# Optimization experiments

Hardware: AMD Instinct MI355X
Metric: run time of the kernel (lower is better)

Reference implementation:

```python
import jax, jax.numpy as jnp
import numpy as np

N_A, N_B, D = 200_000, 400_000, 128
E1, E2 = 800_000, 800_000
UPDATE_KEEP = 0.5   # update_keep_prob
FEAT_KEEP = 0.3     # feature_keep_prob
LN_EPS = 1e-5


def setup_inputs() -> dict:
    key = jax.random.key(0)
    ks = jax.random.split(key, 22)
    s = 0.05  # weight scale
    f32 = jnp.float32
    return {
        "feats_A": jax.random.normal(ks[0], (N_A, D), f32),
        "feats_B": jax.random.normal(ks[1], (N_B, D), f32),
        "W_p2c": jax.random.normal(ks[2], (D, D), f32) * s,
        "b_p2c": jnp.zeros((D,), f32),
        "W_c2p": jax.random.normal(ks[3], (D, D), f32) * s,
        "b_c2p": jnp.zeros((D,), f32),
        "Wself_A": jax.random.normal(ks[4], (D, D), f32) * s,
        "bself_A": jnp.zeros((D,), f32),
        "lnw_A": jnp.ones((D,), f32),
        "lnb_A": jnp.zeros((D,), f32),
        "Wself_B": jax.random.normal(ks[5], (D, D), f32) * s,
        "bself_B": jnp.zeros((D,), f32),
        "lnw_B": jnp.ones((D,), f32),
        "lnb_B": jnp.zeros((D,), f32),
        "u_p2c": jax.random.uniform(ks[6], (E1, 1), f32),
        "u_c2p": jax.random.uniform(ks[7], (E2, 1), f32),
        "u_feat_A": jax.random.uniform(ks[8], (D,), f32),
        "u_feat_B": jax.random.uniform(ks[9], (D,), f32),
        "src_p2c": jax.random.randint(ks[10], (E1,), 0, N_A, jnp.int32),
        "dst_p2c": jax.random.randint(ks[11], (E1,), 0, N_B, jnp.int32),
        "src_c2p": jax.random.randint(ks[12], (E2,), 0, N_B, jnp.int32),
        "dst_c2p": jax.random.randint(ks[13], (E2,), 0, N_A, jnp.int32),
    }


def _edge_aggregate(src_feat, src_idx, dst_idx, W, b, u_edge, n_dst):
    # gather -> per-edge-type linear -> bernoulli update mask -> scatter-add
    msg = src_feat[src_idx] @ W.T + b                     # [E, D]
    um = (u_edge < UPDATE_KEEP).astype(src_feat.dtype)    # [E, 1]
    msg = msg * um
    agg = jax.ops.segment_sum(msg, dst_idx, num_segments=n_dst)       # [n_dst, D]
    deg = jax.ops.segment_sum(um[:, 0], dst_idx, num_segments=n_dst)  # [n_dst]
    return agg, deg


def _table_update(feats, agg, deg, Wself, bself, lnw, lnb, u_feat):
    deg = jnp.maximum(deg, 1.0)[:, None]
    fmask = (u_feat < FEAT_KEEP).astype(feats.dtype)      # [D], bernoulli(0.3)
    agg = (agg / deg) * fmask
    comb = feats @ Wself.T + bself + agg
    mu = jnp.mean(comb, axis=-1, keepdims=True)
    var = jnp.var(comb, axis=-1, keepdims=True)
    comb = (comb - mu) * jax.lax.rsqrt(var + LN_EPS) * lnw + lnb
    comb = jax.nn.selu(comb + feats)                      # residual (Identity proj) + SELU
    # write back only masked feature columns
    return jnp.where(fmask > 0.5, comb, feats)


def reference(feats_A, feats_B, W_p2c, b_p2c, W_c2p, b_c2p,
              Wself_A, bself_A, lnw_A, lnb_A,
              Wself_B, bself_B, lnw_B, lnb_B,
              u_p2c, u_c2p, u_feat_A, u_feat_B,
              src_p2c, dst_p2c, src_c2p, dst_c2p):
    # PARENT_TO_CHILD: A -> B ; CHILD_TO_PARENT: B -> A
    agg_B, deg_B = _edge_aggregate(feats_A, src_p2c, dst_p2c, W_p2c, b_p2c, u_p2c, N_B)
    agg_A, deg_A = _edge_aggregate(feats_B, src_c2p, dst_c2p, W_c2p, b_c2p, u_c2p, N_A)
    out_A = _table_update(feats_A, agg_A, deg_A, Wself_A, bself_A, lnw_A, lnb_A, u_feat_A)
    out_B = _table_update(feats_B, agg_B, deg_B, Wself_B, bself_B, lnw_B, lnb_B, u_feat_B)
    return (out_A, out_B)
```

## Files before the change

### kernel.cpp

```cpp
#include <hip/hip_runtime.h>
#include <hip/hip_bf16.h>

#define DD 128

typedef __attribute__((ext_vector_type(8))) short short8;
typedef __attribute__((ext_vector_type(8))) unsigned short u16x8;
typedef __attribute__((ext_vector_type(4))) unsigned short u16x4;
typedef __attribute__((ext_vector_type(4))) float f32x4;

__device__ __forceinline__ unsigned short f2bf(float f) {
    union { unsigned int u; float f; } c; c.f = f;
    unsigned int u = c.u;
    unsigned int r = (u + 0x7FFFu + ((u >> 16) & 1u)) >> 16;
    return (unsigned short)r;
}
__device__ __forceinline__ float bf2f(unsigned short h) {
    union { unsigned int u; float f; } c; c.u = ((unsigned int)h) << 16; return c.f;
}

__device__ __forceinline__ void scatter_dir(const float* __restrict__ feats,
                                            const int* __restrict__ src,
                                            const int* __restrict__ dst,
                                            const float* __restrict__ u,
                                            unsigned int* __restrict__ pre,
                                            float* __restrict__ deg,
                                            int E, int wave, int lane, int nw)
{
    for (int e = wave; e < E; e += nw) {
        if (u[e] < 0.5f) {
            int s = src[e], d = dst[e];
            float2 x = *(const float2*)(feats + (size_t)s * DD + 2 * lane);
            unsigned int* p = pre + (size_t)d * 64 + lane;
#if defined(__HIP_DEVICE_COMPILE__)
            typedef short sv2 __attribute__((ext_vector_type(2)));
            sv2 v; v[0] = (short)f2bf(x.x); v[1] = (short)f2bf(x.y);
            __builtin_amdgcn_global_atomic_fadd_v2bf16((__attribute__((address_space(1))) sv2*)p, v);
#else
            (void)p; (void)x;
#endif
            if (lane == 0) unsafeAtomicAdd(deg + d, 1.0f);
        }
    }
}

__global__ void scatter2_kernel(const float* __restrict__ f1,
                                const int* __restrict__ s1, const int* __restrict__ d1,
                                const float* __restrict__ u1,
                                unsigned int* __restrict__ p1, float* __restrict__ g1, int E1,
                                const float* __restrict__ f2,
                                const int* __restrict__ s2, const int* __restrict__ d2,
                                const float* __restrict__ u2,
                                unsigned int* __restrict__ p2, float* __restrict__ g2, int E2)
{
    int half = gridDim.x >> 1;
    int lane = threadIdx.x & 63;
    int wavein = (blockIdx.x % half) * (blockDim.x >> 6) + (threadIdx.x >> 6);
    int nw = half * (blockDim.x >> 6);
    if (blockIdx.x < half) scatter_dir(f1, s1, d1, u1, p1, g1, E1, wavein, lane, nw);
    else                   scatter_dir(f2, s2, d2, u2, p2, g2, E2, wavein, lane, nw);
}

__global__ __launch_bounds__(512, 2)
void table_kernel(const float* __restrict__ feats,
                  const unsigned short* __restrict__ pre,
                  const float* __restrict__ deg,
                  const float* __restrict__ Wself,
                  const float* __restrict__ bself,
                  const float* __restrict__ Wedge,
                  const float* __restrict__ bedge,
                  const float* __restrict__ lnw,
                  const float* __restrict__ lnb,
                  const float* __restrict__ ufeat,
                  float* __restrict__ out,
                  int N)
{
    __shared__ __align__(16) unsigned short wlds[2 * 16384];
    __shared__ __align__(16) char xsall[8 * 8192];

    const int tid = threadIdx.x;

    {
        int j  = tid >> 2;
        int kq = tid & 3;
        float fm = ufeat[j] < 0.3f ? 1.0f : 0.0f;
        const float* wsrow = Wself + j * DD + kq * 32;
        const float* werow = Wedge + j * DD + kq * 32;
        char* lbs = (char*)wlds;
        #pragma unroll
        for (int c = 0; c < 4; ++c) {
            unsigned short tS[8], tE[8];
            #pragma unroll
            for (int i = 0; i < 8; ++i) {
                tS[i] = f2bf(wsrow[c * 8 + i]);
                tE[i] = f2bf(werow[c * 8 + i] * fm);
            }
            int addr = (j * 256 + kq * 64 + c * 16) ^ ((j & 7) << 4);
            *(short8*)(lbs + addr)         = *(short8*)tS;
            *(short8*)(lbs + 32768 + addr) = *(short8*)tE;
        }
    }
    __syncthreads();

    const int wave = tid >> 6;
    const int lane = tid & 63;
    const int lj = lane & 15;
    const int lk = lane >> 4;

    float bs[8], bem[8], lw[8], lb[8];
    unsigned fmask = 0;
    #pragma unroll
    for (int ct = 0; ct < 8; ++ct) {
        int col = ct * 16 + lj;
        bool fm = ufeat[col] < 0.3f;
        bs[ct]  = bself[col];
        bem[ct] = fm ? bedge[col] : 0.0f;
        lw[ct]  = lnw[col];
        lb[ct]  = lnb[col];
        fmask |= (fm ? 1u : 0u) << ct;
    }

    char* xs  = xsall + wave * 8192;
    char* ps  = xs + 4096;
    const char* wb = (const char*)wlds;
    const int ldb  = lj * 256 + lk * 16;
    const int xorv = (lj & 7) << 4;

    const int frow = lane >> 5;
    const int fc4  = lane & 31;
    const int prow = lane >> 4;
    const int pch  = lane & 15;

    const int ntiles = N >> 4;
    for (int tile = blockIdx.x * 8 + wave; tile < ntiles; tile += gridDim.x * 8) {
        int row0 = tile << 4;

        #pragma unroll
        for (int j = 0; j < 8; ++j) {
            int row = j * 2 + frow;
            f32x4 v = __builtin_nontemporal_load(
                (const f32x4*)(feats + (size_t)(row0 + row) * DD + fc4 * 4));
            unsigned short t4[4];
            #pragma unroll
            for (int i = 0; i < 4; ++i) t4[i] = f2bf(v[i]);
            *(u16x4*)(xs + row * 256 + ((fc4 * 8) ^ ((row & 7) << 4))) = *(u16x4*)t4;
        }
        #pragma unroll
        for (int c = 0; c < 4; ++c) {
            int row = c * 4 + prow;
            u16x8 v = __builtin_nontemporal_load(
                (const u16x8*)(pre + (size_t)(row0 + row) * DD + pch * 8));
            *(u16x8*)(ps + row * 256 + ((pch * 16) ^ ((row & 7) << 4))) = v;
        }

        float dgr  = deg[row0 + lj];
        float invd = 1.0f / fmaxf(dgr, 1.0f);
        float dpown = dgr > 0.5f ? 1.0f : 0.0f;

        short8 xf[4], pf[4];
        #pragma unroll
        for (int t = 0; t < 4; ++t) {
            int a = (ldb + t * 64) ^ xorv;
            xf[t] = *(const short8*)(xs + a);
            u16x8 pv = *(const u16x8*)(ps + a);
            unsigned short tp[8];
            #pragma unroll
            for (int i = 0; i < 8; ++i) tp[i] = f2bf(bf2f(pv[i]) * invd);
            pf[t] = *(short8*)tp;
        }

        f32x4 acc[8];
        #pragma unroll
        for (int ct = 0; ct < 8; ++ct) { f32x4 z = {0.f,0.f,0.f,0.f}; acc[ct] = z; }

        #pragma unroll
        for (int t = 0; t < 4; ++t) {
            int a0 = (ldb + t * 64) ^ xorv;
            #pragma unroll
            for (int ct = 0; ct < 8; ++ct) {
                short8 ws = *(const short8*)(wb + ct * 4096 + a0);
                short8 we = *(const short8*)(wb + 32768 + ct * 4096 + a0);
                acc[ct] = __builtin_amdgcn_mfma_f32_16x16x32_bf16(xf[t], ws, acc[ct], 0, 0, 0);
                acc[ct] = __builtin_amdgcn_mfma_f32_16x16x32_bf16(pf[t], we, acc[ct], 0, 0, 0);
            }
        }

        #pragma unroll
        for (int q = 0; q < 4; ++q) {
            int rrl = lk * 4 + q;
            float degpos = __shfl(dpown, rrl, 64);
            float val[8];
            float s = 0.f, s2 = 0.f;
            #pragma unroll
            for (int ct = 0; ct < 8; ++ct) {
                float v = acc[ct][q] + bs[ct] + degpos * bem[ct];
                val[ct] = v; s += v; s2 += v * v;
            }
            #pragma unroll
            for (int m = 1; m < 16; m <<= 1) {
                s  += __shfl_xor(s,  m, 64);
                s2 += __shfl_xor(s2, m, 64);
            }
            float mu   = s * (1.0f / 128.0f);
            float var  = s2 * (1.0f / 128.0f) - mu * mu;
            float rstd = rsqrtf(var + 1e-5f);
            #pragma unroll
            for (int ct = 0; ct < 8; ++ct) {
                int col = ct * 16 + lj;
                int ra  = rrl * 256 + ((col * 2) ^ ((rrl & 7) << 4));
                float fres = bf2f(*(const unsigned short*)(xs + ra));
                float ln = (val[ct] - mu) * rstd * lw[ct] + lb[ct];
                float x = ln + fres;
                float selu = x > 0.f ? 1.0507009873554805f * x
                                     : 1.0507009873554805f * 1.6732632423543772f * (expf(x) - 1.0f);
                float o = ((fmask >> ct) & 1) ? selu : fres;
                *(unsigned short*)(xs + ra) = f2bf(o);
            }
        }

        #pragma unroll
        for (int j = 0; j < 8; ++j) {
            int row = j * 2 + frow;
            u16x4 ov = *(const u16x4*)(xs + row * 256 + ((fc4 * 8) ^ ((row & 7) << 4)));
            f32x4 o;
            #pragma unroll
            for (int i = 0; i < 4; ++i) o[i] = bf2f(ov[i]);
            *(f32x4*)(out + (size_t)(row0 + row) * DD + fc4 * 4) = o;
        }
    }
}

extern "C" void kernel_launch(void* const* d_in, const int* in_sizes, int n_in,
                              void* d_out, int out_size, void* d_ws, size_t ws_size,
                              hipStream_t stream)
{
    const float* feats_A = (const float*)d_in[0];
    const float* feats_B = (const float*)d_in[1];
    const float* W_p2c   = (const float*)d_in[2];
    const float* b_p2c   = (const float*)d_in[3];
    const float* W_c2p   = (const float*)d_in[4];
    const float* b_c2p   = (const float*)d_in[5];
    const float* Wself_A = (const float*)d_in[6];
    const float* bself_A = (const float*)d_in[7];
    const float* lnw_A   = (const float*)d_in[8];
    const float* lnb_A   = (const float*)d_in[9];
    const float* Wself_B = (const float*)d_in[10];
    const float* bself_B = (const float*)d_in[11];
    const float* lnw_B   = (const float*)d_in[12];
    const float* lnb_B   = (const float*)d_in[13];
    const float* u_p2c   = (const float*)d_in[14];
    const float* u_c2p   = (const float*)d_in[15];
    const float* u_featA = (const float*)d_in[16];
    const float* u_featB = (const float*)d_in[17];
    const int* src_p2c = (const int*)d_in[18];
    const int* dst_p2c = (const int*)d_in[19];
    const int* src_c2p = (const int*)d_in[20];
    const int* dst_c2p = (const int*)d_in[21];

    const int N_A = in_sizes[0] / DD;
    const int N_B = in_sizes[1] / DD;
    const int E1  = in_sizes[14];
    const int E2  = in_sizes[15];

    float* outA = (float*)d_out;
    float* outB = outA + (size_t)N_A * DD;

    const size_t preB_bytes = (size_t)N_B * DD * 2;
    const size_t preA_bytes = (size_t)N_A * DD * 2;
    const size_t need = preB_bytes + preA_bytes + (size_t)(N_A + N_B) * 4;
    if (ws_size < need) return;

    unsigned int*   preB_w = (unsigned int*)d_ws;
    unsigned int*   preA_w = (unsigned int*)((char*)d_ws + preB_bytes);
    float*          deg_A  = (float*)((char*)d_ws + preB_bytes + preA_bytes);
    float*          deg_B  = deg_A + N_A;
    const unsigned short* preB_h = (const unsigned short*)preB_w;
    const unsigned short* preA_h = (const unsigned short*)preA_w;

    (void)hipMemsetAsync(d_ws, 0, need, stream);

    dim3 sblk(256), sgrd(2048);
    scatter2_kernel<<<sgrd, sblk, 0, stream>>>(feats_A, src_p2c, dst_p2c, u_p2c, preB_w, deg_B, E1,
                                               feats_B, src_c2p, dst_c2p, u_c2p, preA_w, deg_A, E2);

    dim3 tblk(512), tgrd(256);
    table_kernel<<<tgrd, tblk, 0, stream>>>(feats_A, preA_h, deg_A,
                                            Wself_A, bself_A, W_c2p, b_c2p,
                                            lnw_A, lnb_A, u_featA, outA, N_A);
    table_kernel<<<tgrd, tblk, 0, stream>>>(feats_B, preB_h, deg_B,
                                            Wself_B, bself_B, W_p2c, b_p2c,
                                            lnw_B, lnb_B, u_featB, outB, N_B);
}
```

Baseline: 856.5 us.

## Load pre-aggregated rows directly to registers and double waves per table block

The table kernel now runs 1024-thread blocks with 16 waves each. Every wave gets a 4 KB LDS staging area instead of 8 KB, since the pre-aggregated message rows are loaded straight from global memory into MFMA operand registers rather than staged through LDS. The feats loads also switch from nontemporal to normal loads. This cuts LDS traffic and raises the number of resident waves to hide memory latency, at the cost of more register pressure under a tighter launch bound and less coalesced direct loads.

```diff
diff --git a/kernel.cpp b/kernel.cpp
--- a/kernel.cpp
+++ b/kernel.cpp
@@ -60,7 +60,7 @@
     else                   scatter_dir(f2, s2, d2, u2, p2, g2, E2, wavein, lane, nw);
 }
 
-__global__ __launch_bounds__(512, 2)
+__global__ __launch_bounds__(1024, 2)
 void table_kernel(const float* __restrict__ feats,
                   const unsigned short* __restrict__ pre,
                   const float* __restrict__ deg,
@@ -75,26 +75,26 @@
                   int N)
 {
     __shared__ __align__(16) unsigned short wlds[2 * 16384];
-    __shared__ __align__(16) char xsall[8 * 8192];
+    __shared__ __align__(16) char xsall[16 * 4096];
 
     const int tid = threadIdx.x;
 
     {
-        int j  = tid >> 2;
-        int kq = tid & 3;
+        int j   = tid >> 3;
+        int kq8 = tid & 7;
         float fm = ufeat[j] < 0.3f ? 1.0f : 0.0f;
-        const float* wsrow = Wself + j * DD + kq * 32;
-        const float* werow = Wedge + j * DD + kq * 32;
+        const float* wsrow = Wself + j * DD + kq8 * 16;
+        const float* werow = Wedge + j * DD + kq8 * 16;
         char* lbs = (char*)wlds;
         #pragma unroll
-        for (int c = 0; c < 4; ++c) {
+        for (int c = 0; c < 2; ++c) {
             unsigned short tS[8], tE[8];
             #pragma unroll
             for (int i = 0; i < 8; ++i) {
                 tS[i] = f2bf(wsrow[c * 8 + i]);
                 tE[i] = f2bf(werow[c * 8 + i] * fm);
             }
-            int addr = (j * 256 + kq * 64 + c * 16) ^ ((j & 7) << 4);
+            int addr = (j * 256 + kq8 * 32 + c * 16) ^ ((j & 7) << 4);
             *(short8*)(lbs + addr)         = *(short8*)tS;
             *(short8*)(lbs + 32768 + addr) = *(short8*)tE;
         }
@@ -119,52 +119,44 @@
         fmask |= (fm ? 1u : 0u) << ct;
     }
 
-    char* xs  = xsall + wave * 8192;
-    char* ps  = xs + 4096;
+    char* xs = xsall + wave * 4096;
     const char* wb = (const char*)wlds;
     const int ldb  = lj * 256 + lk * 16;
     const int xorv = (lj & 7) << 4;
 
     const int frow = lane >> 5;
     const int fc4  = lane & 31;
-    const int prow = lane >> 4;
-    const int pch  = lane & 15;
 
     const int ntiles = N >> 4;
-    for (int tile = blockIdx.x * 8 + wave; tile < ntiles; tile += gridDim.x * 8) {
+    for (int tile = blockIdx.x * 16 + wave; tile < ntiles; tile += gridDim.x * 16) {
         int row0 = tile << 4;
+        int r = row0 + lj;
 
         #pragma unroll
         for (int j = 0; j < 8; ++j) {
             int row = j * 2 + frow;
-            f32x4 v = __builtin_nontemporal_load(
-                (const f32x4*)(feats + (size_t)(row0 + row) * DD + fc4 * 4));
+            f32x4 v = *(const f32x4*)(feats + (size_t)(row0 + row) * DD + fc4 * 4);
             unsigned short t4[4];
             #pragma unroll
             for (int i = 0; i < 4; ++i) t4[i] = f2bf(v[i]);
             *(u16x4*)(xs + row * 256 + ((fc4 * 8) ^ ((row & 7) << 4))) = *(u16x4*)t4;
         }
-        #pragma unroll
-        for (int c = 0; c < 4; ++c) {
-            int row = c * 4 + prow;
-            u16x8 v = __builtin_nontemporal_load(
-                (const u16x8*)(pre + (size_t)(row0 + row) * DD + pch * 8));
-            *(u16x8*)(ps + row * 256 + ((pch * 16) ^ ((row & 7) << 4))) = v;
-        }
-
-        float dgr  = deg[row0 + lj];
+        u16x8 pv[4];
+        #pragma unroll
+        for (int t = 0; t < 4; ++t)
+            pv[t] = *(const u16x8*)(pre + (size_t)r * DD + t * 32 + lk * 8);
+
+        float dgr  = deg[r];
         float invd = 1.0f / fmaxf(dgr, 1.0f);
         float dpown = dgr > 0.5f ? 1.0f : 0.0f;
 
         short8 xf[4], pf[4];
         #pragma unroll
         for (int t = 0; t < 4; ++t) {
-            int a = (ldb + t * 64) ^ xorv;
-            xf[t] = *(const short8*)(xs + a);
-            u16x8 pv = *(const u16x8*)(ps + a);
+            xf[t] = *(const short8*)(xs + ((ldb + t * 64) ^ xorv));
             unsigned short tp[8];
             #pragma unroll
-            for (int i = 0; i < 8; ++i) tp[i] = f2bf(bf2f(pv[i]) * invd);
+            for (int i = 0; i < 8; ++i) tp[i] = f2bf(bf2f(pv[t][i]) * invd);
             pf[t] = *(short8*)tp;
         }
 
@@ -282,7 +274,7 @@
     scatter2_kernel<<<sgrd, sblk, 0, stream>>>(feats_A, src_p2c, dst_p2c, u_p2c, preB_w, deg_B, E1,
                                                feats_B, src_c2p, dst_c2p, u_c2p, preA_w, deg_A, E2);
 
-    dim3 tblk(512), tgrd(256);
+    dim3 tblk(1024), tgrd(256);
     table_kernel<<<tgrd, tblk, 0, stream>>>(feats_A, preA_h, deg_A,
                                             Wself_A, bself_A, W_c2p, b_c2p,
                                             lnw_A, lnb_A, u_featA, outA, N_A);
```

Result: slower. 1.420 ms (+65.9%).
